# Kernel optimization log

Measured on AMD Instinct MI355X. Metric: run time of the kernel, lower is better.

The kernel has to match this reference:

```python
import jax, jax.numpy as jnp
import numpy as np

EPS = 1e-12  # F.normalize eps


def _gather_nb(var, idx):
    # var: [B, N, C], idx: [B, N, K] -> [B, N, K, C]; out[b,n,k,c] = var[b, idx[b,n,k], c]
    return jnp.take_along_axis(var[:, :, None, :], idx[:, :, :, None], axis=1)


def _l2norm(v):
    n = jnp.sqrt(jnp.sum(v * v, axis=-1, keepdims=True))
    return v / jnp.maximum(n, EPS)


def setup_inputs() -> dict:
    key = jax.random.key(0)
    ks = jax.random.split(key, 16)
    B, N, K, dim, hid = 4, 4096, 16, 128, 64
    s = 0.05
    return {
        "pos": jax.random.normal(ks[0], (B, N, 3), jnp.float32),
        "x": jax.random.normal(ks[1], (B, dim, N), jnp.float32),
        "idx": jax.random.randint(ks[2], (B, N, K), 0, N, jnp.int64),
        "dist": jax.random.uniform(ks[3], (B, N, K), jnp.float32),
        "W_qkv": jax.random.normal(ks[4], (3 * dim, dim), jnp.float32) * s,
        "W1": jax.random.normal(ks[5], (hid, 10), jnp.float32) * s,
        "b1": jax.random.normal(ks[6], (hid,), jnp.float32) * s,
        "W2": jax.random.normal(ks[7], (dim, hid), jnp.float32) * s,
        "b2": jax.random.normal(ks[8], (dim,), jnp.float32) * s,
        "Wm1": jax.random.normal(ks[9], (4 * dim, dim), jnp.float32) * s,
        "bm1": jax.random.normal(ks[10], (4 * dim,), jnp.float32) * s,
        "Wm2": jax.random.normal(ks[11], (dim, 4 * dim), jnp.float32) * s,
        "bm2": jax.random.normal(ks[12], (dim,), jnp.float32) * s,
    }


def reference(pos, x, idx, dist, W_qkv, W1, b1, W2, b2, Wm1, bm1, Wm2, bm2):
    B, _, N = x.shape
    xt = jnp.transpose(x, (0, 2, 1))                      # [B, N, C]
    qkv = xt @ W_qkv.T                                    # [B, N, 3C]
    Q, K_, V = jnp.split(qkv, 3, axis=-1)

    Qg = _gather_nb(Q, idx)                               # [B, N, K, C]
    Kg = _gather_nb(K_, idx)
    Vg = _gather_nb(V, idx)

    # position embedding: [center(3) | neighbor(3) | diff(3) | dist(1)] -> MLP 10->hid->C
    pos_nb = _gather_nb(pos, idx)                         # [B, N, K, 3]
    pos_c = jnp.broadcast_to(pos[:, :, None, :], pos_nb.shape)
    feat10 = jnp.concatenate(
        [pos_c, pos_nb, pos_c - pos_nb, dist[..., None]], axis=-1)  # [B, N, K, 10]
    pos_emb = jax.nn.relu(feat10 @ W1.T + b1) @ W2.T + b2  # [B, N, K, C]

    Knorm = _l2norm(Kg + pos_emb)                         # [B, N, K, C]
    Vrel = jax.nn.relu(Vg + pos_emb)                      # [B, N, K, C]
    Qn = _l2norm(Qg)                                      # [B, N, K, C]

    # kv_context: contract over N per neighbor slot k -> [B, K, C, C]
    kv = jnp.einsum('bnkc,bnkd->bkcd', Knorm, Vrel)
    # (1/N) Qn @ kv, then sum over k -> [B, N, C]
    agg = jnp.einsum('bnkc,bkcd->bnd', Qn, kv) / N

    out = jax.nn.relu(agg @ Wm1.T + bm1) @ Wm2.T + bm2 + xt  # [B, N, C]
    return jnp.transpose(out, (0, 2, 1))                     # [B, C, N]
```

## Files before the change

### kernel.cpp

```cpp
#include <hip/hip_runtime.h>
#include <math.h>

#define Bn 4
#define Nn 4096
#define Kn 16
#define Cn 128
#define HIDn 64

#define OFF_WQKVBF 0
#define OFF_WM1BF  24576
#define OFF_WM2BF  57344
#define OFF_W2BFG  90112
#define OFF_QNBF   94208
#define OFF_KMBF   1142784
#define OFF_VMBF   2191360
#define OFF_KVT32  3239936
#define OFF_KVTBF  4288512
#define OFF_AGG0   4812800
#define OFF_AGG1   6909952
#define OFF_FLAG   9007104

typedef short bf16x8 __attribute__((ext_vector_type(8)));
typedef float f32x4 __attribute__((ext_vector_type(4)));

__device__ inline unsigned short f2bf(float f) {
  union { float f; unsigned u; } v; v.f = f;
  unsigned r = v.u + 0x7fffu + ((v.u >> 16) & 1u);
  return (unsigned short)(r >> 16);
}
__device__ inline float b2f(unsigned short s) {
  union { unsigned u; float f; } v; v.u = ((unsigned)s) << 16; return v.f;
}

__global__ void k0_prep(const float* __restrict__ Wqkv,
                        const float* __restrict__ Wm1, const float* __restrict__ Wm2,
                        const float* __restrict__ W2,
                        const int* __restrict__ idx_raw, float* ws) {
  if (blockIdx.x == 0 && threadIdx.x == 0) {
    int any = 0;
    for (int i = 0; i < 64; ++i) any |= idx_raw[2 * i + 1];
    ((int*)(ws + OFF_FLAG))[0] = (any == 0) ? 1 : 0;
  }
  int t = blockIdx.x * 256 + threadIdx.x;
  if (t < 49152) { ((unsigned short*)(ws + OFF_WQKVBF))[t] = f2bf(Wqkv[t]); return; }
  t -= 49152;
  if (t < 65536) { ((unsigned short*)(ws + OFF_WM1BF))[t] = f2bf(Wm1[t]); return; }
  t -= 65536;
  if (t < 65536) { ((unsigned short*)(ws + OFF_WM2BF))[t] = f2bf(Wm2[t]); return; }
  t -= 65536;
  if (t < 8192) { ((unsigned short*)(ws + OFF_W2BFG))[t] = f2bf(W2[t]); return; }
}

__global__ __launch_bounds__(256, 2) void k1_qkv(const float* __restrict__ x, float* ws) {
  __shared__ __align__(16) unsigned short a_lds[32 * 136];
  __shared__ __align__(16) float qkv_lds[32 * 388];
  const unsigned short* Wq = (const unsigned short*)(ws + OFF_WQKVBF);
  unsigned short* Qnbf = (unsigned short*)(ws + OFF_QNBF);
  unsigned short* KmBF = (unsigned short*)(ws + OFF_KMBF);
  unsigned short* VmBF = (unsigned short*)(ws + OFF_VMBF);
  int b = blockIdx.x >> 7;
  int n0 = (blockIdx.x & 127) << 5;
  int t = threadIdx.x;
  int w = t >> 6, l = t & 63, ml = l & 15, gq = l >> 4;
#pragma unroll
  for (int i = 0; i < 16; ++i) {
    int id = t + 256 * i;
    int c = id >> 5, j = id & 31;
    a_lds[j * 136 + c] = f2bf(x[(b * Cn + c) * Nn + n0 + j]);
  }
  __syncthreads();
  f32x4 acc[2][6];
#pragma unroll
  for (int i = 0; i < 2; ++i)
#pragma unroll
    for (int j = 0; j < 6; ++j) acc[i][j] = (f32x4)0.f;
#pragma unroll
  for (int kc = 0; kc < 4; ++kc) {
    bf16x8 av0 = *(const bf16x8*)&a_lds[ml * 136 + kc * 32 + 8 * gq];
    bf16x8 av1 = *(const bf16x8*)&a_lds[(ml + 16) * 136 + kc * 32 + 8 * gq];
#pragma unroll
    for (int nf = 0; nf < 6; ++nf) {
      int m = 96 * w + 16 * nf + ml;
      bf16x8 bv = *(const bf16x8*)&Wq[m * 128 + kc * 32 + 8 * gq];
      acc[0][nf] = __builtin_amdgcn_mfma_f32_16x16x32_bf16(av0, bv, acc[0][nf], 0, 0, 0);
      acc[1][nf] = __builtin_amdgcn_mfma_f32_16x16x32_bf16(av1, bv, acc[1][nf], 0, 0, 0);
    }
  }
#pragma unroll
  for (int mf = 0; mf < 2; ++mf)
#pragma unroll
    for (int nf = 0; nf < 6; ++nf)
#pragma unroll
      for (int r = 0; r < 4; ++r)
        qkv_lds[(16 * mf + 4 * gq + r) * 388 + 96 * w + 16 * nf + ml] = acc[mf][nf][r];
  __syncthreads();
  {
    int g = t >> 3, l8 = t & 7;
    float4 q4[4];
    float ss = 0.f;
#pragma unroll
    for (int q = 0; q < 4; ++q) {
      q4[q] = *(const float4*)&qkv_lds[g * 388 + l8 * 16 + 4 * q];
      ss = fmaf(q4[q].x, q4[q].x, ss); ss = fmaf(q4[q].y, q4[q].y, ss);
      ss = fmaf(q4[q].z, q4[q].z, ss); ss = fmaf(q4[q].w, q4[q].w, ss);
    }
    ss += __shfl_xor(ss, 1); ss += __shfl_xor(ss, 2); ss += __shfl_xor(ss, 4);
    float sc = 1.f / fmaxf(sqrtf(ss), 1e-12f);
    union { unsigned short us[8]; uint4 u4; } o0, o1;
#pragma unroll
    for (int q = 0; q < 2; ++q) {
      o0.us[q * 4 + 0] = f2bf(q4[q].x * sc); o0.us[q * 4 + 1] = f2bf(q4[q].y * sc);
      o0.us[q * 4 + 2] = f2bf(q4[q].z * sc); o0.us[q * 4 + 3] = f2bf(q4[q].w * sc);
    }
#pragma unroll
    for (int q = 0; q < 2; ++q) {
      o1.us[q * 4 + 0] = f2bf(q4[2 + q].x * sc); o1.us[q * 4 + 1] = f2bf(q4[2 + q].y * sc);
      o1.us[q * 4 + 2] = f2bf(q4[2 + q].z * sc); o1.us[q * 4 + 3] = f2bf(q4[2 + q].w * sc);
    }
    *(uint4*)&Qnbf[(b * Nn + n0 + g) * Cn + l8 * 16] = o0.u4;
    *(uint4*)&Qnbf[(b * Nn + n0 + g) * Cn + l8 * 16 + 8] = o1.u4;
  }
#pragma unroll
  for (int i = 0; i < 2; ++i) {
    int id = t + 256 * i;
    int row = id >> 4, c8 = id & 15;
    const float* kp = &qkv_lds[row * 388 + 128 + c8 * 8];
    const float* vp = &qkv_lds[row * 388 + 256 + c8 * 8];
    union { unsigned short us[8]; uint4 u4; } ko, vo;
#pragma unroll
    for (int j = 0; j < 8; ++j) { ko.us[j] = f2bf(kp[j]); vo.us[j] = f2bf(vp[j]); }
    *(uint4*)&KmBF[(b * Nn + n0 + row) * Cn + c8 * 8] = ko.u4;
    *(uint4*)&VmBF[(b * Nn + n0 + row) * Cn + c8 * 8] = vo.u4;
  }
}

#define CH2 8
__global__ __launch_bounds__(256, 2) void k2_kv(const float* __restrict__ pos,
                                                const float* __restrict__ dist,
                                                const int* __restrict__ idxp,
                                                const float* __restrict__ W1,
                                                const float* __restrict__ b1,
                                                const float* __restrict__ b2,
                                                float* ws) {
  __shared__ __align__(16) unsigned short h_lds[32 * 72];
  __shared__ float pe_lds[32 * 132];
  __shared__ __align__(16) unsigned short K_rm[32 * 136];
  __shared__ __align__(16) unsigned short V_rm[32 * 136];
  __shared__ __align__(16) unsigned short KnT[128 * 40];
  __shared__ __align__(16) unsigned short VrT[128 * 40];
  __shared__ float W1s[640];
  __shared__ float b1s[64];
  __shared__ float b2s[128];

  const unsigned short* KmBF = (const unsigned short*)(ws + OFF_KMBF);
  const unsigned short* VmBF = (const unsigned short*)(ws + OFF_VMBF);
  const unsigned short* W2g = (const unsigned short*)(ws + OFF_W2BFG);
  float* kvt = ws + OFF_KVT32;
  int flag = ((const int*)(ws + OFF_FLAG))[0];

  int bid = blockIdx.x;
  int b = bid & 3;
  int rest = bid >> 2;
  int k = rest & 15, ch = rest >> 4;
  int t = threadIdx.x;
  int w = t >> 6, l = t & 63;
  int ml = l & 15, gq = l >> 4;

  for (int i = t; i < 640; i += 256) W1s[i] = W1[i];
  if (t < 64) b1s[t] = b1[t];
  if (t < 128) b2s[t] = b2[t];

  f32x4 acc[2][8];
#pragma unroll
  for (int i = 0; i < 2; ++i)
#pragma unroll
    for (int j = 0; j < 8; ++j) acc[i][j] = (f32x4)0.f;

  int g = t >> 3, l8 = t & 7;
  int side = t >> 7, cc = t & 127;

  __syncthreads();

  for (int it = 0; it < 16; ++it) {
    int n0 = ch * 512 + it * 32;
    union { unsigned short us[8]; uint4 u4; } ka, kb, va, vb;
    {
      int n = n0 + g;
      int fidx = (b * Nn + n) * Kn + k;
      int jn = flag ? idxp[2 * fidx] : idxp[fidx];
      const unsigned short* krow = &KmBF[(b * Nn + jn) * Cn];
      const unsigned short* vrow = &VmBF[(b * Nn + jn) * Cn];
      ka.u4 = *(const uint4*)&krow[l8 * 16];
      kb.u4 = *(const uint4*)&krow[l8 * 16 + 8];
      va.u4 = *(const uint4*)&vrow[l8 * 16];
      vb.u4 = *(const uint4*)&vrow[l8 * 16 + 8];
      float dd = dist[fidx];
      float pc0 = pos[(b * Nn + n) * 3 + 0], pc1 = pos[(b * Nn + n) * 3 + 1], pc2 = pos[(b * Nn + n) * 3 + 2];
      float pn0 = pos[(b * Nn + jn) * 3 + 0], pn1 = pos[(b * Nn + jn) * 3 + 1], pn2 = pos[(b * Nn + jn) * 3 + 2];
      float f10[10] = {pc0, pc1, pc2, pn0, pn1, pn2, pc0 - pn0, pc1 - pn1, pc2 - pn2, dd};
      union { unsigned short us[8]; uint4 u4; } hv;
#pragma unroll
      for (int oo = 0; oo < 8; ++oo) {
        int o = l8 * 8 + oo;
        float a = b1s[o];
#pragma unroll
        for (int i2 = 0; i2 < 10; ++i2) a = fmaf(W1s[o * 10 + i2], f10[i2], a);
        hv.us[oo] = f2bf(fmaxf(a, 0.f));
      }
      *(uint4*)&h_lds[g * 72 + l8 * 8] = hv.u4;
    }
    __syncthreads();
    {
      f32x4 pacc[2][2];
#pragma unroll
      for (int i = 0; i < 2; ++i)
#pragma unroll
        for (int j = 0; j < 2; ++j) pacc[i][j] = (f32x4)0.f;
#pragma unroll
      for (int hc = 0; hc < 64; hc += 32) {
        bf16x8 av[2];
#pragma unroll
        for (int mf = 0; mf < 2; ++mf)
          av[mf] = *(const bf16x8*)&h_lds[(ml + 16 * mf) * 72 + hc + 8 * gq];
#pragma unroll
        for (int nf = 0; nf < 2; ++nf) {
          int c = 32 * w + 16 * nf + ml;
          bf16x8 bv = *(const bf16x8*)&W2g[c * 64 + hc + 8 * gq];
          pacc[0][nf] = __builtin_amdgcn_mfma_f32_16x16x32_bf16(av[0], bv, pacc[0][nf], 0, 0, 0);
          pacc[1][nf] = __builtin_amdgcn_mfma_f32_16x16x32_bf16(av[1], bv, pacc[1][nf], 0, 0, 0);
        }
      }
#pragma unroll
      for (int mf = 0; mf < 2; ++mf)
#pragma unroll
        for (int nf = 0; nf < 2; ++nf) {
          int c = 32 * w + 16 * nf + ml;
          float b2v = b2s[c];
#pragma unroll
          for (int r = 0; r < 4; ++r)
            pe_lds[(16 * mf + 4 * gq + r) * 132 + c] = pacc[mf][nf][r] + b2v;
        }
    }
    __syncthreads();
    {
      float kr[16], vr[16];
      float ss = 0.f;
#pragma unroll
      for (int q = 0; q < 4; ++q) {
        float4 p = *(const float4*)&pe_lds[g * 132 + l8 * 16 + 4 * q];
        float pv[4] = {p.x, p.y, p.z, p.w};
#pragma unroll
        for (int j2 = 0; j2 < 4; ++j2) {
          int j = 4 * q + j2;
          unsigned short ku = (j < 8) ? ka.us[j] : kb.us[j - 8];
          unsigned short vu = (j < 8) ? va.us[j] : vb.us[j - 8];
          kr[j] = b2f(ku) + pv[j2];
          vr[j] = fmaxf(b2f(vu) + pv[j2], 0.f);
          ss = fmaf(kr[j], kr[j], ss);
        }
      }
      ss += __shfl_xor(ss, 1); ss += __shfl_xor(ss, 2); ss += __shfl_xor(ss, 4);
      float sc = 1.f / fmaxf(sqrtf(ss), 1e-12f);
      union { unsigned short us[8]; uint4 u4; } o;
#pragma unroll
      for (int half = 0; half < 2; ++half) {
#pragma unroll
        for (int j = 0; j < 8; ++j) o.us[j] = f2bf(kr[half * 8 + j] * sc);
        *(uint4*)&K_rm[g * 136 + l8 * 16 + half * 8] = o.u4;
      }
#pragma unroll
      for (int half = 0; half < 2; ++half) {
#pragma unroll
        for (int j = 0; j < 8; ++j) o.us[j] = f2bf(vr[half * 8 + j]);
        *(uint4*)&V_rm[g * 136 + l8 * 16 + half * 8] = o.u4;
      }
    }
    __syncthreads();
    {
      const unsigned short* src = side ? V_rm : K_rm;
      unsigned short* dst = side ? VrT : KnT;
      unsigned v[16];
#pragma unroll
      for (int i = 0; i < 16; ++i) {
        unsigned lo = src[(2 * i) * 136 + cc];
        unsigned hi = src[(2 * i + 1) * 136 + cc];
        v[i] = lo | (hi << 16);
      }
#pragma unroll
      for (int i = 0; i < 4; ++i) {
        uint4 pk = {v[4 * i], v[4 * i + 1], v[4 * i + 2], v[4 * i + 3]};
        *(uint4*)&dst[cc * 40 + 8 * i] = pk;
      }
    }
    __syncthreads();
    {
      bf16x8 av[2];
#pragma unroll
      for (int mf = 0; mf < 2; ++mf)
        av[mf] = *(const bf16x8*)&VrT[(32 * w + 16 * mf + ml) * 40 + 8 * gq];
#pragma unroll
      for (int nf = 0; nf < 8; ++nf) {
        bf16x8 bv = *(const bf16x8*)&KnT[(16 * nf + ml) * 40 + 8 * gq];
#pragma unroll
        for (int mf = 0; mf < 2; ++mf)
          acc[mf][nf] = __builtin_amdgcn_mfma_f32_16x16x32_bf16(av[mf], bv, acc[mf][nf], 0, 0, 0);
      }
    }
  }
  float* kvp = kvt + (b * Kn + k) * Cn * Cn;
#pragma unroll
  for (int mf = 0; mf < 2; ++mf)
#pragma unroll
    for (int nf = 0; nf < 8; ++nf) {
      int c = 16 * nf + ml;
#pragma unroll
      for (int r = 0; r < 4; ++r) {
        int d = 32 * w + 16 * mf + 4 * gq + r;
        atomicAdd(&kvp[d * Cn + c], acc[mf][nf][r]);
      }
    }
}

__global__ __launch_bounds__(256) void k2b_cvt(float* ws) {
  const float* src = ws + OFF_KVT32;
  unsigned short* dst = (unsigned short*)(ws + OFF_KVTBF);
  int i = blockIdx.x * 256 + threadIdx.x;
  float4 a = *(const float4*)&src[i * 8];
  float4 c = *(const float4*)&src[i * 8 + 4];
  union { unsigned short us[8]; uint4 u4; } o;
  o.us[0] = f2bf(a.x); o.us[1] = f2bf(a.y); o.us[2] = f2bf(a.z); o.us[3] = f2bf(a.w);
  o.us[4] = f2bf(c.x); o.us[5] = f2bf(c.y); o.us[6] = f2bf(c.z); o.us[7] = f2bf(c.w);
  *(uint4*)&dst[i * 8] = o.u4;
}

__global__ __launch_bounds__(256, 4) void k3_agg(const int* __restrict__ idxp, float* ws) {
  __shared__ __align__(16) unsigned short qt[32 * 136];
  const unsigned short* Qnbf = (const unsigned short*)(ws + OFF_QNBF);
  const unsigned short* kvtbf = (const unsigned short*)(ws + OFF_KVTBF);
  int flag = ((const int*)(ws + OFF_FLAG))[0];

  int bid = blockIdx.x;
  int b = bid & 3;
  int kh = (bid >> 2) & 1;
  int nt = bid >> 3;
  int n0 = nt * 32;
  int t = threadIdx.x;
  int w = t >> 6, l = t & 63;
  int ml = l & 15, gq = l >> 4;

  f32x4 acc[2][2];
#pragma unroll
  for (int i = 0; i < 2; ++i)
#pragma unroll
    for (int j = 0; j < 2; ++j) acc[i][j] = (f32x4)0.f;

  for (int kk = 0; kk < 8; ++kk) {
    int k = kh * 8 + kk;
    __syncthreads();
#pragma unroll
    for (int i = 0; i < 2; ++i) {
      int id = t + 256 * i;
      int row = id >> 4, c16 = id & 15;
      int fidx = (b * Nn + n0 + row) * Kn + k;
      int jn = flag ? idxp[2 * fidx] : idxp[fidx];
      uint4 v = *(const uint4*)&Qnbf[(b * Nn + jn) * Cn + c16 * 8];
      *(uint4*)&qt[row * 136 + c16 * 8] = v;
    }
    __syncthreads();
    const unsigned short* kvp = &kvtbf[(b * Kn + k) * Cn * Cn];
#pragma unroll
    for (int c0 = 0; c0 < 128; c0 += 32) {
      bf16x8 a0 = *(const bf16x8*)&qt[ml * 136 + c0 + 8 * gq];
      bf16x8 a1 = *(const bf16x8*)&qt[(ml + 16) * 136 + c0 + 8 * gq];
#pragma unroll
      for (int nf = 0; nf < 2; ++nf) {
        int d = 32 * w + 16 * nf + ml;
        bf16x8 bv = *(const bf16x8*)&kvp[d * Cn + c0 + 8 * gq];
        acc[0][nf] = __builtin_amdgcn_mfma_f32_16x16x32_bf16(a0, bv, acc[0][nf], 0, 0, 0);
        acc[1][nf] = __builtin_amdgcn_mfma_f32_16x16x32_bf16(a1, bv, acc[1][nf], 0, 0, 0);
      }
    }
  }
  float* ag = ws + (kh ? OFF_AGG1 : OFF_AGG0);
#pragma unroll
  for (int mf = 0; mf < 2; ++mf)
#pragma unroll
    for (int nf = 0; nf < 2; ++nf) {
      int d = 32 * w + 16 * nf + ml;
#pragma unroll
      for (int r = 0; r < 4; ++r) {
        int n = n0 + 16 * mf + 4 * gq + r;
        ag[(b * Nn + n) * Cn + d] = acc[mf][nf][r];
      }
    }
}

__global__ __launch_bounds__(256, 2) void k4_mlp(const float* __restrict__ x,
                                                 const float* __restrict__ bm1,
                                                 const float* __restrict__ bm2,
                                                 float* __restrict__ out, float* ws) {
  __shared__ __align__(16) unsigned short a_lds[32 * 136];
  __shared__ __align__(16) unsigned short h_lds[32 * 520];
  __shared__ float out_s[128 * 33];
  const float* agg0 = ws + OFF_AGG0;
  const float* agg1 = ws + OFF_AGG1;
  const unsigned short* Wm1bf = (const unsigned short*)(ws + OFF_WM1BF);
  const unsigned short* Wm2bf = (const unsigned short*)(ws + OFF_WM2BF);
  const float invN = 1.f / (float)Nn;
  int b = blockIdx.x >> 7;
  int n0 = (blockIdx.x & 127) << 5;
  int t = threadIdx.x;
  int w = t >> 6, l = t & 63, ml = l & 15, gq = l >> 4;
#pragma unroll
  for (int i = 0; i < 4; ++i) {
    int id = t + 256 * i;
    int row = id >> 5, c4 = id & 31;
    int off = (b * Nn + n0 + row) * Cn + c4 * 4;
    float4 v0 = *(const float4*)&agg0[off];
    float4 v1 = *(const float4*)&agg1[off];
    union { unsigned short us[4]; uint2 u2; } o;
    o.us[0] = f2bf((v0.x + v1.x) * invN); o.us[1] = f2bf((v0.y + v1.y) * invN);
    o.us[2] = f2bf((v0.z + v1.z) * invN); o.us[3] = f2bf((v0.w + v1.w) * invN);
    *(uint2*)&a_lds[row * 136 + c4 * 4] = o.u2;
  }
  __syncthreads();
  {
    f32x4 hacc[2][8];
#pragma unroll
    for (int i = 0; i < 2; ++i)
#pragma unroll
      for (int j = 0; j < 8; ++j) hacc[i][j] = (f32x4)0.f;
#pragma unroll
    for (int kc = 0; kc < 4; ++kc) {
      bf16x8 av0 = *(const bf16x8*)&a_lds[ml * 136 + kc * 32 + 8 * gq];
      bf16x8 av1 = *(const bf16x8*)&a_lds[(ml + 16) * 136 + kc * 32 + 8 * gq];
#pragma unroll
      for (int nf = 0; nf < 8; ++nf) {
        int h = 128 * w + 16 * nf + ml;
        bf16x8 bv = *(const bf16x8*)&Wm1bf[h * 128 + kc * 32 + 8 * gq];
        hacc[0][nf] = __builtin_amdgcn_mfma_f32_16x16x32_bf16(av0, bv, hacc[0][nf], 0, 0, 0);
        hacc[1][nf] = __builtin_amdgcn_mfma_f32_16x16x32_bf16(av1, bv, hacc[1][nf], 0, 0, 0);
      }
    }
#pragma unroll
    for (int mf = 0; mf < 2; ++mf)
#pragma unroll
      for (int nf = 0; nf < 8; ++nf) {
        int h = 128 * w + 16 * nf + ml;
        float bias = bm1[h];
#pragma unroll
        for (int r = 0; r < 4; ++r)
          h_lds[(16 * mf + 4 * gq + r) * 520 + h] = f2bf(fmaxf(hacc[mf][nf][r] + bias, 0.f));
      }
  }
  __syncthreads();
  {
    f32x4 oacc[2][2];
#pragma unroll
    for (int i = 0; i < 2; ++i)
#pragma unroll
      for (int j = 0; j < 2; ++j) oacc[i][j] = (f32x4)0.f;
#pragma unroll
    for (int kc = 0; kc < 16; ++kc) {
      bf16x8 av0 = *(const bf16x8*)&h_lds[ml * 520 + kc * 32 + 8 * gq];
      bf16x8 av1 = *(const bf16x8*)&h_lds[(ml + 16) * 520 + kc * 32 + 8 * gq];
#pragma unroll
      for (int nf = 0; nf < 2; ++nf) {
        int co = 32 * w + 16 * nf + ml;
        bf16x8 bv = *(const bf16x8*)&Wm2bf[co * 512 + kc * 32 + 8 * gq];
        oacc[0][nf] = __builtin_amdgcn_mfma_f32_16x16x32_bf16(av0, bv, oacc[0][nf], 0, 0, 0);
        oacc[1][nf] = __builtin_amdgcn_mfma_f32_16x16x32_bf16(av1, bv, oacc[1][nf], 0, 0, 0);
      }
    }
#pragma unroll
    for (int mf = 0; mf < 2; ++mf)
#pragma unroll
      for (int nf = 0; nf < 2; ++nf) {
        int co = 32 * w + 16 * nf + ml;
        float bias = bm2[co];
#pragma unroll
        for (int r = 0; r < 4; ++r)
          out_s[co * 33 + 16 * mf + 4 * gq + r] = oacc[mf][nf][r] + bias;
      }
  }
  __syncthreads();
#pragma unroll
  for (int i = 0; i < 16; ++i) {
    int id = t + 256 * i;
    int co = id >> 5, j = id & 31;
    out[(b * Cn + co) * Nn + n0 + j] = out_s[co * 33 + j] + x[(b * Cn + co) * Nn + n0 + j];
  }
}

extern "C" void kernel_launch(void* const* d_in, const int* in_sizes, int n_in,
                              void* d_out, int out_size, void* d_ws, size_t ws_size,
                              hipStream_t stream) {
  const float* pos  = (const float*)d_in[0];
  const float* x    = (const float*)d_in[1];
  const int*   idx  = (const int*)d_in[2];
  const float* dist = (const float*)d_in[3];
  const float* Wqkv = (const float*)d_in[4];
  const float* W1   = (const float*)d_in[5];
  const float* b1   = (const float*)d_in[6];
  const float* W2   = (const float*)d_in[7];
  const float* b2   = (const float*)d_in[8];
  const float* Wm1  = (const float*)d_in[9];
  const float* bm1  = (const float*)d_in[10];
  const float* Wm2  = (const float*)d_in[11];
  const float* bm2  = (const float*)d_in[12];
  float* out = (float*)d_out;
  float* ws = (float*)d_ws;

  hipMemsetAsync(ws + OFF_KVT32, 0, (size_t)Bn * Kn * Cn * Cn * sizeof(float), stream);
  hipLaunchKernelGGL(k0_prep, dim3(736), dim3(256), 0, stream, Wqkv, Wm1, Wm2, W2, idx, ws);
  hipLaunchKernelGGL(k1_qkv, dim3(Bn * 128), dim3(256), 0, stream, x, ws);
  hipLaunchKernelGGL(k2_kv, dim3(Bn * Kn * CH2), dim3(256), 0, stream, pos, dist, idx, W1, b1, b2, ws);
  hipLaunchKernelGGL(k2b_cvt, dim3(512), dim3(256), 0, stream, ws);
  hipLaunchKernelGGL(k3_agg, dim3(Bn * 2 * 128), dim3(256), 0, stream, idx, ws);
  hipLaunchKernelGGL(k4_mlp, dim3(Bn * 128), dim3(256), 0, stream, x, bm1, bm2, out, ws);
}
```

Measured before the change: 179.9 us.

## Prefetch next iteration's neighbor gathers in k2_kv and shrink LDS usage

The k2_kv loop now software-pipelines its global gathers. Indices, dist, positions and the K/V bf16 rows for the next 32-point chunk are loaded during the current iteration, so gather latency overlaps with the MFMA work. The position embedding is staged in LDS as bf16 instead of fp32. The W1, b1 and b2 copies in LDS are dropped in favour of direct global reads, and threads are remapped so each wave owns its own rows in the K/V norm stage. The changes aim to hide memory latency and cut LDS footprint for better occupancy, at the cost of more registers, extra rounding of pos_emb to bf16, and redundant reads of W1 and b2 from global/cache.

Result: faster. 167.2 us (-7.0%).

```diff
diff --git a/kernel.cpp b/kernel.cpp
--- a/kernel.cpp
+++ b/kernel.cpp
@@ -143,14 +143,11 @@
                                                 const float* __restrict__ b2,
                                                 float* ws) {
   __shared__ __align__(16) unsigned short h_lds[32 * 72];
-  __shared__ float pe_lds[32 * 132];
+  __shared__ __align__(16) unsigned short pe_bf[32 * 136];
   __shared__ __align__(16) unsigned short K_rm[32 * 136];
   __shared__ __align__(16) unsigned short V_rm[32 * 136];
   __shared__ __align__(16) unsigned short KnT[128 * 40];
   __shared__ __align__(16) unsigned short VrT[128 * 40];
-  __shared__ float W1s[640];
-  __shared__ float b1s[64];
-  __shared__ float b2s[128];
 
   const unsigned short* KmBF = (const unsigned short*)(ws + OFF_KMBF);
   const unsigned short* VmBF = (const unsigned short*)(ws + OFF_VMBF);
@@ -166,9 +163,10 @@
   int w = t >> 6, l = t & 63;
   int ml = l & 15, gq = l >> 4;
 
-  for (int i = t; i < 640; i += 256) W1s[i] = W1[i];
-  if (t < 64) b1s[t] = b1[t];
-  if (t < 128) b2s[t] = b2[t];
+  int g = t >> 3, l8 = t & 7;
+  int nl = (t >> 3) & 7, half = t & 7;
+  int n_b2 = 8 * w + nl;
+  int side = t >> 7, cc = t & 127;
 
   f32x4 acc[2][8];
 #pragma unroll
@@ -176,39 +174,50 @@
 #pragma unroll
     for (int j = 0; j < 8; ++j) acc[i][j] = (f32x4)0.f;
 
-  int g = t >> 3, l8 = t & 7;
-  int side = t >> 7, cc = t & 127;
-
-  __syncthreads();
+  int nbase = ch * 512;
+  int fidx_m = (b * Nn + nbase + g) * Kn + k;
+  int jn_m = flag ? idxp[2 * fidx_m] : idxp[fidx_m];
+  float dd = dist[fidx_m];
+  float pc0 = pos[(b * Nn + nbase + g) * 3 + 0];
+  float pc1 = pos[(b * Nn + nbase + g) * 3 + 1];
+  float pc2 = pos[(b * Nn + nbase + g) * 3 + 2];
+  float pn0 = pos[(b * Nn + jn_m) * 3 + 0];
+  float pn1 = pos[(b * Nn + jn_m) * 3 + 1];
+  float pn2 = pos[(b * Nn + jn_m) * 3 + 2];
+  int fidx_b = (b * Nn + nbase + n_b2) * Kn + k;
+  int jn_b = flag ? idxp[2 * fidx_b] : idxp[fidx_b];
+  union U8 { unsigned short us[8]; uint4 u4; };
+  U8 ka, kb, va, vb;
+  {
+    const unsigned short* krow = &KmBF[(b * Nn + jn_b) * Cn];
+    const unsigned short* vrow = &VmBF[(b * Nn + jn_b) * Cn];
+    ka.u4 = *(const uint4*)&krow[half * 16];
+    kb.u4 = *(const uint4*)&krow[half * 16 + 8];
+    va.u4 = *(const uint4*)&vrow[half * 16];
+    vb.u4 = *(const uint4*)&vrow[half * 16 + 8];
+  }
 
   for (int it = 0; it < 16; ++it) {
-    int n0 = ch * 512 + it * 32;
-    union { unsigned short us[8]; uint4 u4; } ka, kb, va, vb;
     {
-      int n = n0 + g;
-      int fidx = (b * Nn + n) * Kn + k;
-      int jn = flag ? idxp[2 * fidx] : idxp[fidx];
-      const unsigned short* krow = &KmBF[(b * Nn + jn) * Cn];
-      const unsigned short* vrow = &VmBF[(b * Nn + jn) * Cn];
-      ka.u4 = *(const uint4*)&krow[l8 * 16];
-      kb.u4 = *(const uint4*)&krow[l8 * 16 + 8];
-      va.u4 = *(const uint4*)&vrow[l8 * 16];
-      vb.u4 = *(const uint4*)&vrow[l8 * 16 + 8];
-      float dd = dist[fidx];
-      float pc0 = pos[(b * Nn + n) * 3 + 0], pc1 = pos[(b * Nn + n) * 3 + 1], pc2 = pos[(b * Nn + n) * 3 + 2];
-      float pn0 = pos[(b * Nn + jn) * 3 + 0], pn1 = pos[(b * Nn + jn) * 3 + 1], pn2 = pos[(b * Nn + jn) * 3 + 2];
       float f10[10] = {pc0, pc1, pc2, pn0, pn1, pn2, pc0 - pn0, pc1 - pn1, pc2 - pn2, dd};
       union { unsigned short us[8]; uint4 u4; } hv;
 #pragma unroll
       for (int oo = 0; oo < 8; ++oo) {
         int o = l8 * 8 + oo;
-        float a = b1s[o];
-#pragma unroll
-        for (int i2 = 0; i2 < 10; ++i2) a = fmaf(W1s[o * 10 + i2], f10[i2], a);
+        float a = b1[o];
+#pragma unroll
+        for (int i2 = 0; i2 < 10; ++i2) a = fmaf(W1[o * 10 + i2], f10[i2], a);
         hv.us[oo] = f2bf(fmaxf(a, 0.f));
       }
       *(uint4*)&h_lds[g * 72 + l8 * 8] = hv.u4;
     }
+    int itn = (it < 15) ? it + 1 : 15;
+    int n0n = nbase + itn * 32;
+    int fidx_mn = (b * Nn + n0n + g) * Kn + k;
+    int jn_mn = flag ? idxp[2 * fidx_mn] : idxp[fidx_mn];
+    float ddn = dist[fidx_mn];
+    int fidx_bn = (b * Nn + n0n + n_b2) * Kn + k;
+    int jn_bn = flag ? idxp[2 * fidx_bn] : idxp[fidx_bn];
     __syncthreads();
     {
       f32x4 pacc[2][2];
@@ -235,45 +244,63 @@
 #pragma unroll
         for (int nf = 0; nf < 2; ++nf) {
           int c = 32 * w + 16 * nf + ml;
-          float b2v = b2s[c];
 #pragma unroll
           for (int r = 0; r < 4; ++r)
-            pe_lds[(16 * mf + 4 * gq + r) * 132 + c] = pacc[mf][nf][r] + b2v;
+            pe_bf[(16 * mf + 4 * gq + r) * 136 + c] = f2bf(pacc[mf][nf][r]);
         }
     }
     __syncthreads();
     {
+      U8 pa, pb;
+      pa.u4 = *(const uint4*)&pe_bf[n_b2 * 136 + half * 16];
+      pb.u4 = *(const uint4*)&pe_bf[n_b2 * 136 + half * 16 + 8];
+      const float4* b2v4 = (const float4*)b2;
+      float4 bz[4];
+#pragma unroll
+      for (int q = 0; q < 4; ++q) bz[q] = b2v4[half * 4 + q];
       float kr[16], vr[16];
       float ss = 0.f;
 #pragma unroll
-      for (int q = 0; q < 4; ++q) {
-        float4 p = *(const float4*)&pe_lds[g * 132 + l8 * 16 + 4 * q];
-        float pv[4] = {p.x, p.y, p.z, p.w};
-#pragma unroll
-        for (int j2 = 0; j2 < 4; ++j2) {
-          int j = 4 * q + j2;
-          unsigned short ku = (j < 8) ? ka.us[j] : kb.us[j - 8];
-          unsigned short vu = (j < 8) ? va.us[j] : vb.us[j - 8];
-          kr[j] = b2f(ku) + pv[j2];
-          vr[j] = fmaxf(b2f(vu) + pv[j2], 0.f);
-          ss = fmaf(kr[j], kr[j], ss);
-        }
+      for (int j = 0; j < 16; ++j) {
+        float b2j = (j & 2) ? ((j & 1) ? bz[j >> 2].w : bz[j >> 2].z)
+                            : ((j & 1) ? bz[j >> 2].y : bz[j >> 2].x);
+        float pe = b2f((j < 8) ? pa.us[j] : pb.us[j - 8]) + b2j;
+        float kg = b2f((j < 8) ? ka.us[j] : kb.us[j - 8]);
+        float vg = b2f((j < 8) ? va.us[j] : vb.us[j - 8]);
+        kr[j] = kg + pe;
+        vr[j] = fmaxf(vg + pe, 0.f);
+        ss = fmaf(kr[j], kr[j], ss);
       }
       ss += __shfl_xor(ss, 1); ss += __shfl_xor(ss, 2); ss += __shfl_xor(ss, 4);
       float sc = 1.f / fmaxf(sqrtf(ss), 1e-12f);
       union { unsigned short us[8]; uint4 u4; } o;
 #pragma unroll
-      for (int half = 0; half < 2; ++half) {
-#pragma unroll
-        for (int j = 0; j < 8; ++j) o.us[j] = f2bf(kr[half * 8 + j] * sc);
-        *(uint4*)&K_rm[g * 136 + l8 * 16 + half * 8] = o.u4;
-      }
-#pragma unroll
-      for (int half = 0; half < 2; ++half) {
-#pragma unroll
-        for (int j = 0; j < 8; ++j) o.us[j] = f2bf(vr[half * 8 + j]);
-        *(uint4*)&V_rm[g * 136 + l8 * 16 + half * 8] = o.u4;
-      }
+      for (int hh = 0; hh < 2; ++hh) {
+#pragma unroll
+        for (int j = 0; j < 8; ++j) o.us[j] = f2bf(kr[hh * 8 + j] * sc);
+        *(uint4*)&K_rm[n_b2 * 136 + half * 16 + 8 * hh] = o.u4;
+      }
+#pragma unroll
+      for (int hh = 0; hh < 2; ++hh) {
+#pragma unroll
+        for (int j = 0; j < 8; ++j) o.us[j] = f2bf(vr[hh * 8 + j]);
+        *(uint4*)&V_rm[n_b2 * 136 + half * 16 + 8 * hh] = o.u4;
+      }
+    }
+    float pc0n = pos[(b * Nn + n0n + g) * 3 + 0];
+    float pc1n = pos[(b * Nn + n0n + g) * 3 + 1];
+    float pc2n = pos[(b * Nn + n0n + g) * 3 + 2];
+    float pn0n = pos[(b * Nn + jn_mn) * 3 + 0];
+    float pn1n = pos[(b * Nn + jn_mn) * 3 + 1];
+    float pn2n = pos[(b * Nn + jn_mn) * 3 + 2];
+    U8 kan, kbn, van, vbn;
+    {
+      const unsigned short* krow = &KmBF[(b * Nn + jn_bn) * Cn];
+      const unsigned short* vrow = &VmBF[(b * Nn + jn_bn) * Cn];
+      kan.u4 = *(const uint4*)&krow[half * 16];
+      kbn.u4 = *(const uint4*)&krow[half * 16 + 8];
+      van.u4 = *(const uint4*)&vrow[half * 16];
+      vbn.u4 = *(const uint4*)&vrow[half * 16 + 8];
     }
     __syncthreads();
     {
@@ -306,6 +333,10 @@
           acc[mf][nf] = __builtin_amdgcn_mfma_f32_16x16x32_bf16(av[mf], bv, acc[mf][nf], 0, 0, 0);
       }
     }
+    dd = ddn;
+    pc0 = pc0n; pc1 = pc1n; pc2 = pc2n;
+    pn0 = pn0n; pn1 = pn1n; pn2 = pn2n;
+    ka.u4 = kan.u4; kb.u4 = kbn.u4; va.u4 = van.u4; vb.u4 = vbn.u4;
   }
   float* kvp = kvt + (b * Kn + k) * Cn * Cn;
 #pragma unroll
```
